# Performance work log

Measured on AMD Instinct MI355X. Metric: run time of the kernel, lower is better.

## Reference

```python
import jax, jax.numpy as jnp
import numpy as np

B, N, D = 8, 2048, 512
S = 4096  # max_swaps


def setup_inputs() -> dict:
    key = jax.random.key(0)
    ks = jax.random.split(key, 5)
    h = jax.random.normal(ks[0], (B, N, D), dtype=jnp.float32)
    indices = jax.random.randint(ks[1], (B, S, 4), 0, N, dtype=jnp.int64)
    # MLP params (Linear stores weight as (out,in) in torch; we keep (in,out) and matmul)
    W1 = jax.random.normal(ks[2], (4 * D, D), dtype=jnp.float32) * (1.0 / np.sqrt(4 * D))
    b1 = jnp.zeros((D,), dtype=jnp.float32)
    W2 = jax.random.normal(ks[3], (D, D // 2), dtype=jnp.float32) * (1.0 / np.sqrt(D))
    b2 = jnp.zeros((D // 2,), dtype=jnp.float32)
    W3 = jax.random.normal(ks[4], (D // 2, 1), dtype=jnp.float32) * (1.0 / np.sqrt(D // 2))
    b3 = jnp.zeros((1,), dtype=jnp.float32)
    return {"h": h, "indices": indices, "W1": W1, "b1": b1, "W2": W2, "b2": b2, "W3": W3, "b3": b3}


def reference(h, indices, W1, b1, W2, b2, W3, b3):
    # h: (B, N, D); indices: (B, S, 4) node ids per swap
    swap_emb = jnp.take_along_axis(h[:, None, :, :], indices[..., None].astype(jnp.int32),
                                   axis=2)  # broadcast-gather -> (B, S, 4, D)
    # equivalently: h[batch_idx, indices]; implemented as per-batch gather
    swap_emb = jax.vmap(lambda hb, ib: hb[ib])(h, indices)  # (B, S, 4, D)
    swap_feats = swap_emb.reshape(h.shape[0], indices.shape[1], -1)  # (B, S, 4D)
    x = jax.nn.gelu(swap_feats @ W1 + b1, approximate=False)
    x = jax.nn.gelu(x @ W2 + b2, approximate=False)
    scores = (x @ W3 + b3)[..., 0]  # (B, S)
    rates = jax.nn.softplus(scores)
    return rates
```

## Files before the change

### kernel.cpp

```cpp
#include <hip/hip_runtime.h>
#include <math.h>

#define BATCH 8
#define NNODES 2048
#define DDIM 512
#define SWAPS 4096
#define M_TOTAL (BATCH * SWAPS)
#define KD DDIM
#define K2 DDIM
#define N2 (DDIM / 2)

typedef __attribute__((ext_vector_type(8))) __bf16 bf16x8;
typedef __attribute__((ext_vector_type(4))) float f32x4;
typedef __attribute__((ext_vector_type(8))) unsigned short us8;
typedef unsigned short ushort_t;

__device__ __forceinline__ float gelu_fast(float x) {
    const float u = 0.7978845608028654f * x * fmaf(0.044715f * x, x, 1.0f);
    const float e = __expf(-2.0f * fabsf(u));
    float t = (1.0f - e) / (1.0f + e);
    t = copysignf(t, u);
    return 0.5f * x * (1.0f + t);
}
__device__ __forceinline__ float softplus_f(float x) {
    return fmaxf(x, 0.0f) + log1pf(expf(-fabsf(x)));
}
__device__ __forceinline__ unsigned short f2bf(float f) {
    unsigned int u = __builtin_bit_cast(unsigned int, f);
    u += 0x7FFFu + ((u >> 16) & 1u);
    return (unsigned short)(u >> 16);
}
__device__ __forceinline__ float bf2f(unsigned short s) {
    return __builtin_bit_cast(float, (unsigned int)s << 16);
}
__device__ __forceinline__ void glds16(const void* g, void* l) {
    __builtin_amdgcn_global_load_lds(
        (const __attribute__((address_space(1))) void*)g,
        (__attribute__((address_space(3))) void*)l, 16, 0, 0);
}

__global__ __launch_bounds__(256) void convert_kernel(
    const float* __restrict__ h, const float* __restrict__ W1,
    const float* __restrict__ W2, ushort_t* __restrict__ h_bf,
    ushort_t* __restrict__ W1pt, ushort_t* __restrict__ W2f)
{
    const int bid = blockIdx.x;
    const int tid = threadIdx.x;
    if (bid < 4096) {
        const size_t i = ((size_t)bid * 256 + tid) * 8;
        float4 v0 = *(const float4*)(h + i);
        float4 v1 = *(const float4*)(h + i + 4);
        us8 o;
        o[0] = f2bf(v0.x); o[1] = f2bf(v0.y); o[2] = f2bf(v0.z); o[3] = f2bf(v0.w);
        o[4] = f2bf(v1.x); o[5] = f2bf(v1.y); o[6] = f2bf(v1.z); o[7] = f2bf(v1.w);
        *(us8*)(h_bf + i) = o;
    } else if (bid < 4096 + 256) {
        __shared__ ushort_t sT[64][72];
        const int tb = bid - 4096;
        const int kt = tb >> 3, nt = tb & 7;
        const int kl = tid >> 4;
        const int n4 = (tid & 15) * 4;
        #pragma unroll
        for (int p = 0; p < 4; ++p) {
            const int k_local = p * 16 + kl;
            float4 v = *(const float4*)(W1 + (size_t)(kt * 64 + k_local) * 512
                                        + nt * 64 + n4);
            sT[n4 + 0][k_local] = f2bf(v.x);
            sT[n4 + 1][k_local] = f2bf(v.y);
            sT[n4 + 2][k_local] = f2bf(v.z);
            sT[n4 + 3][k_local] = f2bf(v.w);
        }
        __syncthreads();
        const int n_local = tid >> 2, ch = tid & 3;
        const int j = (kt >> 3) * 512 + nt * 64 + n_local;
        const int d0 = (kt & 7) * 64 + ch * 16;
        us8 o0, o1;
        #pragma unroll
        for (int e = 0; e < 8; ++e) { o0[e] = sT[n_local][ch * 16 + e];
                                      o1[e] = sT[n_local][ch * 16 + 8 + e]; }
        *(us8*)(W1pt + (size_t)j * KD + d0)     = o0;
        *(us8*)(W1pt + (size_t)j * KD + d0 + 8) = o1;
    } else {
        size_t e = ((size_t)(bid - 4352) * 256 + tid) * 4;
        const int k = (int)(e >> 8), n = (int)(e & 255);
        const int kc = k >> 5, quad = (k >> 3) & 3, pos = k & 7;
        const size_t base = (size_t)kc * 8192 + quad * 8 + pos;
        float4 v = *(const float4*)(W2 + e);
        W2f[base + (size_t)(n + 0) * 32] = f2bf(v.x);
        W2f[base + (size_t)(n + 1) * 32] = f2bf(v.y);
        W2f[base + (size_t)(n + 2) * 32] = f2bf(v.z);
        W2f[base + (size_t)(n + 3) * 32] = f2bf(v.w);
    }
}

__global__ __launch_bounds__(256) void gemm1_dense(
    const ushort_t* __restrict__ h_bf, const ushort_t* __restrict__ W1pt,
    ushort_t* __restrict__ P2)
{
    __shared__ __align__(16) char smem[32768];

    const int tid = threadIdx.x;
    const int w = tid >> 6, lane = tid & 63;
    const int quad = lane >> 4, l16 = lane & 15;
    const int wr = w >> 1, wc = w & 1;

    const int bid = blockIdx.x;
    const int xcd = bid & 7;
    const int r = bid >> 3;
    const int m0 = xcd * NNODES + (r & 15) * 128;
    const int n0 = (r >> 4) * 128;

    const int row0 = tid >> 2, sub = tid & 3;
    const int cg = (sub - (row0 >> 1)) & 3;
    const ushort_t* bA0 = h_bf + (size_t)(m0 + row0) * KD + cg * 8;
    const ushort_t* bA1 = h_bf + (size_t)(m0 + row0 + 64) * KD + cg * 8;
    const ushort_t* bB0 = W1pt + (size_t)(n0 + row0) * KD + cg * 8;
    const ushort_t* bB1 = W1pt + (size_t)(n0 + row0 + 64) * KD + cg * 8;

    int pa[4], pb[4];
    #pragma unroll
    for (int i = 0; i < 4; ++i) {
        const int rA = wr * 64 + i * 16 + l16;
        const int rB = wc * 64 + i * 16 + l16;
        pa[i] = rA * 64 + (((quad + (rA >> 1)) & 3) * 16);
        pb[i] = 8192 + rB * 64 + (((quad + (rB >> 1)) & 3) * 16);
    }

    f32x4 acc[4][4] = {};

    auto stage = [&](int kt, int half) {
        const int oo = kt * 32;
        char* base = smem + half * 16384;
        glds16(bA0 + oo, base + w * 1024);
        glds16(bA1 + oo, base + 4096 + w * 1024);
        glds16(bB0 + oo, base + 8192 + w * 1024);
        glds16(bB1 + oo, base + 12288 + w * 1024);
    };
    auto compute = [&](int half) {
        const char* base = smem + half * 16384;
        bf16x8 af[4], bfr[4];
        #pragma unroll
        for (int i = 0; i < 4; ++i) {
            af[i]  = *(const bf16x8*)(base + pa[i]);
            bfr[i] = *(const bf16x8*)(base + pb[i]);
        }
        #pragma unroll
        for (int i = 0; i < 4; ++i)
            #pragma unroll
            for (int jj = 0; jj < 4; ++jj)
                acc[i][jj] = __builtin_amdgcn_mfma_f32_16x16x32_bf16(
                    af[i], bfr[jj], acc[i][jj], 0, 0, 0);
    };

    for (int kt = 0; kt < 16; kt += 2) {
        stage(kt, 0);
        stage(kt + 1, 1);
        __syncthreads();
        compute(0);
        compute(1);
        __syncthreads();
    }

    #pragma unroll
    for (int jj = 0; jj < 4; ++jj) {
        const int j = n0 + wc * 64 + jj * 16 + l16;
        const int sg = j >> 9, nh = j & 511;
        const size_t base = ((size_t)(xcd * 2 + (nh >> 8)) * NNODES) * 1024
                          + (size_t)(sg << 8) + (nh & 255);
        #pragma unroll
        for (int i = 0; i < 4; ++i) {
            f32x4 v = acc[i][jj];
            #pragma unroll
            for (int rr = 0; rr < 4; ++rr) {
                const int node = (m0 + wr * 64 + i * 16 + quad * 4 + rr) & (NNODES - 1);
                P2[base + (size_t)node * 1024] = f2bf(v[rr]);
            }
        }
    }
}

__global__ __launch_bounds__(512) void fused_tail(
    const ushort_t* __restrict__ P2, const int* __restrict__ idx,
    const float* __restrict__ b1, const ushort_t* __restrict__ W2f,
    const float* __restrict__ b2, const float* __restrict__ W3,
    const float* __restrict__ b3, float* __restrict__ out)
{
    __shared__ __align__(16) char smem[66560];

    const int tid = threadIdx.x;
    const int w = tid >> 6, lane = tid & 63;
    const int quad = lane >> 4, l16 = lane & 15;

    const int bid = blockIdx.x;
    const int b = bid & 7;
    const int m0 = b * SWAPS + (bid >> 3) * 64;

    {
        const int row = tid >> 3;
        const int ws  = tid & 7;
        const int ap  = ws & 3;
        const int ncs = ws >> 2;
        const int acg = (ap - (row >> 1)) & 3;
        const int4 iv = *(const int4*)(idx + (size_t)(m0 + row) * 4);
        const ushort_t* Pr = P2 + (size_t)(b * 2 + ncs) * NNODES * 1024;
        const ushort_t* p0 = Pr + (size_t)iv.x * 1024 + 0 * 256;
        const ushort_t* p1 = Pr + (size_t)iv.y * 1024 + 1 * 256;
        const ushort_t* p2 = Pr + (size_t)iv.z * 1024 + 2 * 256;
        const ushort_t* p3 = Pr + (size_t)iv.w * 1024 + 3 * 256;
        #pragma unroll 4
        for (int it = 0; it < 8; ++it) {
            const int kc = ncs * 8 + it;
            const int pos0 = it * 32 + acg * 8;
            us8 v0 = *(const us8*)(p0 + pos0);
            us8 v1 = *(const us8*)(p1 + pos0);
            us8 v2 = *(const us8*)(p2 + pos0);
            us8 v3 = *(const us8*)(p3 + pos0);
            const float* bp = b1 + ncs * 256 + pos0;
            float4 ba = *(const float4*)bp;
            float4 bb = *(const float4*)(bp + 4);
            float s[8] = { ba.x, ba.y, ba.z, ba.w, bb.x, bb.y, bb.z, bb.w };
            #pragma unroll
            for (int e = 0; e < 8; ++e)
                s[e] += bf2f(v0[e]) + bf2f(v1[e]) + bf2f(v2[e]) + bf2f(v3[e]);
            us8 o;
            #pragma unroll
            for (int e = 0; e < 8; ++e) o[e] = f2bf(gelu_fast(s[e]));
            *(us8*)(smem + kc * 4096 + row * 64 + ap * 16) = o;
        }
    }
    __syncthreads();

    const int rg = w >> 2, cg = w & 3;
    int paRow[2];
    #pragma unroll
    for (int i = 0; i < 2; ++i) {
        const int rA = rg * 32 + i * 16 + l16;
        paRow[i] = rA * 64 + (((quad + (rA >> 1)) & 3) * 16);
    }
    const ushort_t* Bbase = W2f + (size_t)(cg * 64 + l16) * 32 + quad * 8;

    f32x4 acc[2][4] = {};

    #pragma unroll 2
    for (int kc = 0; kc < 16; ++kc) {
        bf16x8 af0 = *(const bf16x8*)(smem + kc * 4096 + paRow[0]);
        bf16x8 af1 = *(const bf16x8*)(smem + kc * 4096 + paRow[1]);
        #pragma unroll
        for (int jf = 0; jf < 4; ++jf) {
            bf16x8 bfr = *(const bf16x8*)(Bbase + (size_t)kc * 8192 + jf * 512);
            acc[0][jf] = __builtin_amdgcn_mfma_f32_16x16x32_bf16(af0, bfr, acc[0][jf], 0, 0, 0);
            acc[1][jf] = __builtin_amdgcn_mfma_f32_16x16x32_bf16(af1, bfr, acc[1][jf], 0, 0, 0);
        }
    }

    float part[2][4] = {};
    #pragma unroll
    for (int jf = 0; jf < 4; ++jf) {
        const int n = cg * 64 + jf * 16 + l16;
        const float w3 = W3[n];
        const float bb2 = b2[n];
        #pragma unroll
        for (int i = 0; i < 2; ++i) {
            f32x4 v = acc[i][jf];
            #pragma unroll
            for (int rr = 0; rr < 4; ++rr)
                part[i][rr] = fmaf(gelu_fast(v[rr] + bb2), w3, part[i][rr]);
        }
    }
    #pragma unroll
    for (int off = 1; off < 16; off <<= 1)
        #pragma unroll
        for (int i = 0; i < 2; ++i)
            #pragma unroll
            for (int rr = 0; rr < 4; ++rr)
                part[i][rr] += __shfl_xor(part[i][rr], off);

    float* red = (float*)(smem + 65536);
    if (l16 == 0) {
        #pragma unroll
        for (int i = 0; i < 2; ++i)
            #pragma unroll
            for (int rr = 0; rr < 4; ++rr)
                red[cg * 64 + rg * 32 + i * 16 + quad * 4 + rr] = part[i][rr];
    }
    __syncthreads();
    if (tid < 64) {
        const float v = red[tid] + red[64 + tid] + red[128 + tid] + red[192 + tid];
        out[m0 + tid] = softplus_f(v + b3[0]);
    }
}

extern "C" void kernel_launch(void* const* d_in, const int* in_sizes, int n_in,
                              void* d_out, int out_size, void* d_ws, size_t ws_size,
                              hipStream_t stream) {
    const float* h   = (const float*)d_in[0];
    const int*   idx = (const int*)d_in[1];
    const float* W1  = (const float*)d_in[2];
    const float* b1  = (const float*)d_in[3];
    const float* W2  = (const float*)d_in[4];
    const float* b2  = (const float*)d_in[5];
    const float* W3  = (const float*)d_in[6];
    const float* b3  = (const float*)d_in[7];
    float* out = (float*)d_out;

    char* ws = (char*)d_ws;
    ushort_t* P2    = (ushort_t*)ws;
    ushort_t* h_bf  = (ushort_t*)(ws + (64u << 20));
    ushort_t* W1pt  = (ushort_t*)(ws + (80u << 20));
    ushort_t* W2f   = (ushort_t*)(ws + (82u << 20));

    convert_kernel<<<4480, 256, 0, stream>>>(h, W1, W2, h_bf, W1pt, W2f);
    gemm1_dense<<<2048, 256, 0, stream>>>(h_bf, W1pt, P2);
    fused_tail<<<512, 512, 0, stream>>>(P2, idx, b1, W2f, b2, W3, b3, out);
}
```

Measured before the change: 169.8 us.

## Enlarge gemm1 tiles to 256x256 with 4-stage async LDS pipeline

Rewrites the dense first GEMM to use 256x256 output tiles per 512-thread block instead of 128x128 per 256-thread block. It adds a 4-slot LDS ring (128KB) with 3 tiles prefetched, split A/B staging interleaved with MFMA phases, explicit vmcnt waits and raw barriers, and s_setprio around the MFMA bursts. The aim is more operand reuse per load and better overlap of global-to-LDS traffic with compute. In exchange it uses far more LDS per block, which may allow only one block per CU, and the hand-counted vmcnt synchronization is fragile.

```diff
diff --git a/kernel.cpp b/kernel.cpp
--- a/kernel.cpp
+++ b/kernel.cpp
@@ -93,86 +93,115 @@
     }
 }
 
-__global__ __launch_bounds__(256) void gemm1_dense(
+__global__ __launch_bounds__(512, 2) void gemm1_dense(
     const ushort_t* __restrict__ h_bf, const ushort_t* __restrict__ W1pt,
     ushort_t* __restrict__ P2)
 {
-    __shared__ __align__(16) char smem[32768];
+    __shared__ __align__(16) char smem[131072];
 
     const int tid = threadIdx.x;
     const int w = tid >> 6, lane = tid & 63;
     const int quad = lane >> 4, l16 = lane & 15;
-    const int wr = w >> 1, wc = w & 1;
+    const int wr = w >> 2, wc = w & 3;
 
     const int bid = blockIdx.x;
     const int xcd = bid & 7;
     const int r = bid >> 3;
-    const int m0 = xcd * NNODES + (r & 15) * 128;
-    const int n0 = (r >> 4) * 128;
-
-    const int row0 = tid >> 2, sub = tid & 3;
-    const int cg = (sub - (row0 >> 1)) & 3;
-    const ushort_t* bA0 = h_bf + (size_t)(m0 + row0) * KD + cg * 8;
-    const ushort_t* bA1 = h_bf + (size_t)(m0 + row0 + 64) * KD + cg * 8;
-    const ushort_t* bB0 = W1pt + (size_t)(n0 + row0) * KD + cg * 8;
-    const ushort_t* bB1 = W1pt + (size_t)(n0 + row0 + 64) * KD + cg * 8;
-
-    int pa[4], pb[4];
-    #pragma unroll
-    for (int i = 0; i < 4; ++i) {
-        const int rA = wr * 64 + i * 16 + l16;
-        const int rB = wc * 64 + i * 16 + l16;
-        pa[i] = rA * 64 + (((quad + (rA >> 1)) & 3) * 16);
-        pb[i] = 8192 + rB * 64 + (((quad + (rB >> 1)) & 3) * 16);
-    }
-
-    f32x4 acc[4][4] = {};
-
-    auto stage = [&](int kt, int half) {
-        const int oo = kt * 32;
-        char* base = smem + half * 16384;
-        glds16(bA0 + oo, base + w * 1024);
-        glds16(bA1 + oo, base + 4096 + w * 1024);
-        glds16(bB0 + oo, base + 8192 + w * 1024);
-        glds16(bB1 + oo, base + 12288 + w * 1024);
+    const int m0 = xcd * NNODES + (r & 7) * 256;
+    const int n0 = (r >> 3) * 256;
+
+    const int srow = tid >> 2;
+    const int cg = ((tid & 3) - (srow >> 1)) & 3;
+    const ushort_t* srcA = h_bf + (size_t)(m0 + srow) * KD + cg * 8;
+    const ushort_t* srcB = W1pt + (size_t)(n0 + srow) * KD + cg * 8;
+    char* dstBase = smem + w * 1024;
+
+    int paOff[8], pbOff[4];
+    #pragma unroll
+    for (int mi = 0; mi < 8; ++mi) {
+        const int rA = wr * 128 + mi * 16 + l16;
+        paOff[mi] = rA * 64 + (((quad + (rA >> 1)) & 3) * 16);
+    }
+    #pragma unroll
+    for (int jf = 0; jf < 4; ++jf) {
+        const int rB = wc * 64 + jf * 16 + l16;
+        pbOff[jf] = 16384 + rB * 64 + (((quad + (rB >> 1)) & 3) * 16);
+    }
+
+    f32x4 acc[8][4] = {};
+
+    auto stageA = [&](int t3) {
+        const int slotOff = (t3 & 3) * 32768;
+        const ushort_t* s0 = srcA + t3 * 32;
+        glds16(s0,         dstBase + slotOff);
+        glds16(s0 + 65536, dstBase + slotOff + 8192);
     };
-    auto compute = [&](int half) {
-        const char* base = smem + half * 16384;
-        bf16x8 af[4], bfr[4];
-        #pragma unroll
-        for (int i = 0; i < 4; ++i) {
-            af[i]  = *(const bf16x8*)(base + pa[i]);
-            bfr[i] = *(const bf16x8*)(base + pb[i]);
-        }
-        #pragma unroll
-        for (int i = 0; i < 4; ++i)
-            #pragma unroll
-            for (int jj = 0; jj < 4; ++jj)
-                acc[i][jj] = __builtin_amdgcn_mfma_f32_16x16x32_bf16(
-                    af[i], bfr[jj], acc[i][jj], 0, 0, 0);
+    auto stageB = [&](int t3) {
+        const int slotOff = (t3 & 3) * 32768;
+        const ushort_t* s0 = srcB + t3 * 32;
+        glds16(s0,         dstBase + slotOff + 16384);
+        glds16(s0 + 65536, dstBase + slotOff + 24576);
     };
 
-    for (int kt = 0; kt < 16; kt += 2) {
-        stage(kt, 0);
-        stage(kt + 1, 1);
-        __syncthreads();
-        compute(0);
-        compute(1);
-        __syncthreads();
-    }
-
-    #pragma unroll
-    for (int jj = 0; jj < 4; ++jj) {
-        const int j = n0 + wc * 64 + jj * 16 + l16;
+    auto tileBody = [&](int t, bool doStage) {
+        const char* sp = smem + (t & 3) * 32768;
+        bf16x8 bq[4], af[4];
+        #pragma unroll
+        for (int jf = 0; jf < 4; ++jf) bq[jf] = *(const bf16x8*)(sp + pbOff[jf]);
+        #pragma unroll
+        for (int mi = 0; mi < 4; ++mi) af[mi] = *(const bf16x8*)(sp + paOff[mi]);
+        if (doStage) stageA(t + 3);
+        __builtin_amdgcn_s_barrier();
+        __builtin_amdgcn_s_setprio(1);
+        #pragma unroll
+        for (int mi = 0; mi < 4; ++mi)
+            #pragma unroll
+            for (int jf = 0; jf < 4; ++jf)
+                acc[mi][jf] = __builtin_amdgcn_mfma_f32_16x16x32_bf16(
+                    af[mi], bq[jf], acc[mi][jf], 0, 0, 0);
+        __builtin_amdgcn_s_setprio(0);
+        #pragma unroll
+        for (int mi = 0; mi < 4; ++mi) af[mi] = *(const bf16x8*)(sp + paOff[4 + mi]);
+        if (doStage) stageB(t + 3);
+        __builtin_amdgcn_s_barrier();
+        __builtin_amdgcn_s_setprio(1);
+        #pragma unroll
+        for (int mi = 0; mi < 4; ++mi)
+            #pragma unroll
+            for (int jf = 0; jf < 4; ++jf)
+                acc[4 + mi][jf] = __builtin_amdgcn_mfma_f32_16x16x32_bf16(
+                    af[mi], bq[jf], acc[4 + mi][jf], 0, 0, 0);
+        __builtin_amdgcn_s_setprio(0);
+    };
+
+    stageA(0); stageB(0);
+    stageA(1); stageB(1);
+    stageA(2); stageB(2);
+
+    for (int t = 0; t < 14; ++t) {
+        asm volatile("s_waitcnt vmcnt(8)" ::: "memory");
+        __builtin_amdgcn_s_barrier();
+        tileBody(t, t < 13);
+    }
+    asm volatile("s_waitcnt vmcnt(4)" ::: "memory");
+    __builtin_amdgcn_s_barrier();
+    tileBody(14, false);
+    asm volatile("s_waitcnt vmcnt(0)" ::: "memory");
+    __builtin_amdgcn_s_barrier();
+    tileBody(15, false);
+
+    #pragma unroll
+    for (int jf = 0; jf < 4; ++jf) {
+        const int j = n0 + wc * 64 + jf * 16 + l16;
         const int sg = j >> 9, nh = j & 511;
         const size_t base = ((size_t)(xcd * 2 + (nh >> 8)) * NNODES) * 1024
                           + (size_t)(sg << 8) + (nh & 255);
         #pragma unroll
-        for (int i = 0; i < 4; ++i) {
-            f32x4 v = acc[i][jj];
+        for (int mi = 0; mi < 8; ++mi) {
+            f32x4 v = acc[mi][jf];
             #pragma unroll
             for (int rr = 0; rr < 4; ++rr) {
-                const int node = (m0 + wr * 64 + i * 16 + quad * 4 + rr) & (NNODES - 1);
+                const int node = (m0 + wr * 128 + mi * 16 + quad * 4 + rr) & (NNODES - 1);
                 P2[base + (size_t)node * 1024] = f2bf(v[rr]);
             }
         }
@@ -310,6 +339,6 @@
     ushort_t* W2f   = (ushort_t*)(ws + (82u << 20));
 
     convert_kernel<<<4480, 256, 0, stream>>>(h, W1, W2, h_bf, W1pt, W2f);
-    gemm1_dense<<<2048, 256, 0, stream>>>(h_bf, W1pt, P2);
+    gemm1_dense<<<512, 512, 0, stream>>>(h_bf, W1pt, P2);
     fused_tail<<<512, 512, 0, stream>>>(P2, idx, b1, W2f, b2, W3, b3, out);
 }
```

Result: no change. 173.1 us (+2.0%).
